# Kernel tuning notes

Measured on AMD Instinct MI355X. Metric: run time of the kernel, lower is better.

## Reference

```python
import jax, jax.numpy as jnp
import numpy as np

BEAM_WIDTH = 16   # beam_width init kwarg
TOP_PATHS = 1     # top_paths init kwarg
NEG = -1.0e30     # log-domain 'zero' (avoid -inf for stable grads)


def _beam_search_single(log_probs):
    """CTC prefix beam search for one example.

    log_probs: (T, V) log-softmax scores; blank is class V-1 (TF convention).
    Returns (decoded, scores): decoded (TOP_PATHS, T) int32 padded with -1,
    scores (TOP_PATHS,) final log-probabilities of the top prefixes.
    Prefix merging is done for the blank/repeat (stay) transitions of each
    beam (the dominant merge in CTC); cross-beam duplicate-prefix merging is
    approximated by pruning, as in common production beam-search kernels.
    """
    T, V = log_probs.shape
    C = V - 1                      # number of non-blank characters
    W = BEAM_WIDTH

    prefixes = jnp.full((W, T), -1, dtype=jnp.int32)
    lengths = jnp.zeros((W,), dtype=jnp.int32)
    p_b = jnp.full((W,), NEG, dtype=log_probs.dtype).at[0].set(0.0)   # log P(prefix, ends in blank)
    p_nb = jnp.full((W,), NEG, dtype=log_probs.dtype)                 # log P(prefix, ends in non-blank)

    def step(state, lp):
        prefixes, lengths, p_b, p_nb = state
        lp_blank = lp[C]
        lp_c = lp[:C]                                   # (C,)
        p_tot = jnp.logaddexp(p_b, p_nb)                # (W,)

        # last character of each beam (-1 if empty prefix)
        last = jnp.take_along_axis(prefixes, jnp.maximum(lengths - 1, 0)[:, None], axis=1)[:, 0]
        last = jnp.where(lengths > 0, last, -1)

        # --- stay candidates: same prefix, via blank or repeated last char ---
        new_p_b = p_tot + lp_blank                      # (W,)
        lp_last = jnp.take(lp_c, jnp.maximum(last, 0))
        new_p_nb_stay = jnp.where(last >= 0, p_nb + lp_last, NEG)
        stay_score = jnp.logaddexp(new_p_b, new_p_nb_stay)

        # --- extend candidates: prefix + c, for every non-blank c ---
        same = jnp.arange(C)[None, :] == last[:, None]  # (W, C)
        base = jnp.where(same, p_b[:, None], p_tot[:, None])
        ext_score = base + lp_c[None, :]                # (W, C) -> new p_nb

        all_scores = jnp.concatenate([stay_score, ext_score.reshape(-1)])  # (W + W*C,)
        top_scores, top_idx = jax.lax.top_k(all_scores, W)

        is_stay = top_idx < W
        beam = jnp.where(is_stay, top_idx, (top_idx - W) // C)
        char = jnp.where(is_stay, 0, (top_idx - W) % C).astype(jnp.int32)

        par_pref = prefixes[beam]                       # (W, T)
        par_len = lengths[beam]                         # (W,)
        pos = jnp.arange(T)[None, :]
        ext_pref = jnp.where(pos == par_len[:, None], char[:, None], par_pref)

        new_prefixes = jnp.where(is_stay[:, None], par_pref, ext_pref)
        new_lengths = jnp.where(is_stay, par_len, par_len + 1)
        new_pb = jnp.where(is_stay, new_p_b[beam], NEG)
        new_pnb = jnp.where(is_stay, new_p_nb_stay[beam], top_scores)
        return (new_prefixes, new_lengths, new_pb, new_pnb), None

    (prefixes, lengths, p_b, p_nb), _ = jax.lax.scan(step, (prefixes, lengths, p_b, p_nb), log_probs)

    final_scores = jnp.logaddexp(p_b, p_nb)             # (W,)
    best_scores, best_idx = jax.lax.top_k(final_scores, TOP_PATHS)
    return prefixes[best_idx], best_scores


def setup_inputs() -> dict:
    key = jax.random.key(0)
    # (batch, time, num_classes) logits, blank = last class (TF convention)
    inputs = jax.random.normal(key, (512, 512, 96), dtype=jnp.float32)
    return {"inputs": inputs}


def reference(inputs):
    # tf.nn.ctc_beam_search_decoder normalizes logits internally
    log_probs = jax.nn.log_softmax(inputs, axis=-1)        # (B, T, V)
    decoded, scores = jax.vmap(_beam_search_single)(log_probs)
    # decoded: (B, TOP_PATHS, T) token ids padded with -1 (stands in for the
    # string-table detokenize); probability = exp(log_probability) as in call()
    probability = jnp.exp(scores)                          # (B, TOP_PATHS)
    return decoded, probability
```

## Files before the change

### kernel.cpp

```cpp
#include <hip/hip_runtime.h>
#include <math.h>

#define NBATCH 512
#define TSTEPS 512
#define VCLS   96
#define CCLS   95
#define BWID   16
#define VPAD   104
#define NEGF   (-1e30f)

typedef unsigned long long u64;
typedef unsigned int u32;

__device__ __forceinline__ float exp_xla(float x){
    x = fminf(x, 88.3762626647950f);
    x = fmaxf(x, -88.3762626647949f);
    float t = __fadd_rn(__fmul_rn(x, 1.44269504088896341f), 0.5f);
    float m = floorf(t);
    float r = __fadd_rn(__fmul_rn(m, -0.693359375f), x);
    r = __fadd_rn(__fmul_rn(m, 2.12194440e-4f), r);
    float y = 1.9875691500E-4f;
    y = __fadd_rn(__fmul_rn(y, r), 1.3981999507E-3f);
    y = __fadd_rn(__fmul_rn(y, r), 8.3334519073E-3f);
    y = __fadd_rn(__fmul_rn(y, r), 4.1665795894E-2f);
    y = __fadd_rn(__fmul_rn(y, r), 1.6666665459E-1f);
    y = __fadd_rn(__fmul_rn(y, r), 5.0000001201E-1f);
    float r2 = __fmul_rn(r, r);
    y = __fadd_rn(__fmul_rn(y, r2), r);
    y = __fadd_rn(y, 1.0f);
    int n = (int)m;
    unsigned sb = (unsigned)(n + 127);
    float s = __uint_as_float(sb << 23);
    return __fmul_rn(y, s);
}

__device__ __forceinline__ float log_xla(float x){
    unsigned bits = __float_as_uint(x);
    int e = (int)(bits >> 23) - 126;
    float m = __uint_as_float((bits & 0x007FFFFFu) | 0x3F000000u);
    if (m < 0.707106781186547524f){
        e -= 1;
        m = __fsub_rn(__fadd_rn(m, m), 1.0f);
    } else {
        m = __fsub_rn(m, 1.0f);
    }
    float z = __fmul_rn(m, m);
    float p = 7.0376836292E-2f;
    p = __fadd_rn(__fmul_rn(p, m), -1.1514610310E-1f);
    p = __fadd_rn(__fmul_rn(p, m),  1.1676998740E-1f);
    p = __fadd_rn(__fmul_rn(p, m), -1.2420140846E-1f);
    p = __fadd_rn(__fmul_rn(p, m),  1.4249322787E-1f);
    p = __fadd_rn(__fmul_rn(p, m), -1.6668057665E-1f);
    p = __fadd_rn(__fmul_rn(p, m),  2.0000714765E-1f);
    p = __fadd_rn(__fmul_rn(p, m), -2.4999993993E-1f);
    p = __fadd_rn(__fmul_rn(p, m),  3.3333331174E-1f);
    float y = __fmul_rn(m, __fmul_rn(z, p));
    float fe = (float)e;
    y = __fadd_rn(y, __fmul_rn(-2.12194440e-4f, fe));
    y = __fadd_rn(y, __fmul_rn(-0.5f, z));
    float rr = __fadd_rn(m, y);
    rr = __fadd_rn(rr, __fmul_rn(0.693359375f, fe));
    return rr;
}

__device__ __forceinline__ float log1p_xla(float x){
    float u = __fadd_rn(x, 1.0f);
    if (u == 1.0f) return x;
    float lu = log_xla(u);
    float um1 = __fsub_rn(u, 1.0f);
    return __fmul_rn(lu, __fdiv_rn(x, um1));
}

__device__ __forceinline__ float logaddexp_x(float x, float y){
    float amax = fmaxf(x, y);
    float d = __fsub_rn(x, y);
    float e = exp_xla(-fabsf(d));
    float l1p = log1p_xla(e);
    return __fadd_rn(amax, l1p);
}

__device__ __forceinline__ unsigned ford(float f){
    unsigned u = __float_as_uint(f);
    return (u & 0x80000000u) ? ~u : (u | 0x80000000u);
}
__device__ __forceinline__ float unford(u32 u){
    return __uint_as_float((u & 0x80000000u) ? (u ^ 0x80000000u) : ~u);
}

__device__ __forceinline__ double packkey(float sc, int k){
    u64 kb = ((u64)ford(sc) << 31) | ((u64)((~(u32)k) & 0x7FFu) << 20);
    return __longlong_as_double((long long)kb);
}
__device__ __forceinline__ int decodekey(double wk){
    u32 idxinv = (u32)((u64)__double_as_longlong(wk) >> 20) & 0x7FFu;
    return (int)((~idxinv) & 0x7FFu);
}
__device__ __forceinline__ double packlp(float v, int c){
    u64 kb = ((u64)ford(v) << 31) | ((u64)((~(u32)c) & 0x7Fu) << 24);
    return __longlong_as_double((long long)kb);
}

__device__ __forceinline__ void wave_fence(){
    asm volatile("s_waitcnt lgkmcnt(0)" ::: "memory");
    __builtin_amdgcn_sched_barrier(0);
}

template<int CTRL>
__device__ __forceinline__ double dmaxd(double v){
    long long x = __double_as_longlong(v);
    int lo = __builtin_amdgcn_update_dpp((int)(u32)x, (int)(u32)x, CTRL, 0xF, 0xF, false);
    int hi = __builtin_amdgcn_update_dpp((int)(u32)(x >> 32), (int)(u32)(x >> 32), CTRL, 0xF, 0xF, false);
    double o = __longlong_as_double((long long)(((u64)(u32)hi << 32) | (u32)lo));
    return fmax(v, o);
}
template<int CTRL>
__device__ __forceinline__ float dmaxf(float v){
    int o = __builtin_amdgcn_update_dpp(__float_as_int(v), __float_as_int(v), CTRL, 0xF, 0xF, false);
    return fmaxf(v, __int_as_float(o));
}
__device__ __forceinline__ double rowmax_d(double v){
    v = dmaxd<0xB1>(v);
    v = dmaxd<0x4E>(v);
    v = dmaxd<0x141>(v);
    v = dmaxd<0x140>(v);
    return v;
}
__device__ __forceinline__ float rowmax_f(float v){
    v = dmaxf<0xB1>(v);
    v = dmaxf<0x4E>(v);
    v = dmaxf<0x141>(v);
    v = dmaxf<0x140>(v);
    return v;
}

__global__ __launch_bounds__(128)
void ctc_beam(const float* __restrict__ in, float* __restrict__ out)
{
    __shared__ __align__(16) float ring[8][2][VPAD];
    __shared__ __align__(8)  float2 srtS[8][2][17];
    __shared__ __align__(16) float evS[4][VPAD];
    __shared__ float lsS[4];
    __shared__ float2 stateF2[2][BWID];
    __shared__ int2   lastlenS[2][BWID];
    __shared__ unsigned short bp[2][TSTEPS][BWID];
    __shared__ float finalsS[2][BWID];

    const int tid  = threadIdx.x;
    const int wid  = tid >> 6;
    const int lane = tid & 63;
    const int rl   = lane & 15;
    const int eh   = (lane >> 4) & 1;
    const int bm   = rl;
    const int unit = lane >> 4;
    const int pex  = unit & 1;
    const int pdt  = unit >> 1;
    const int bex  = blockIdx.x * 2 + eh;
    const int pbex = blockIdx.x * 2 + pex;
    const float* __restrict__ prow = in + (size_t)pbex * TSTEPS * VCLS;

    float pb_r = NEGF, pnb_r = NEGF;
    int last_r = -1, len_r = 0;

    float xv[6], xw[6];

    auto LOADROW = [&](int r, float* dst){
        const float* p = prow + (size_t)r * VCLS + rl;
        #pragma unroll
        for (int j = 0; j < 6; ++j) dst[j] = p[j * 16];
    };
    auto PRODUCE = [&](int buf, const float* x){
        float lm = fmaxf(fmaxf(fmaxf(x[0], x[1]), fmaxf(x[2], x[3])), fmaxf(x[4], x[5]));
        float m = rowmax_f(lm);
        float sh[6];
        #pragma unroll
        for (int j = 0; j < 6; ++j){
            sh[j] = __fsub_rn(x[j], m);
            evS[unit][j * 16 + rl] = exp_xla(sh[j]);
        }
        wave_fence();
        if (rl == 0){
            float s = 0.0f;
            const float4* e4 = (const float4*)evS[unit];
            #pragma unroll
            for (int g = 0; g < 24; ++g){
                float4 w = e4[g];
                s = __fadd_rn(s, w.x); s = __fadd_rn(s, w.y);
                s = __fadd_rn(s, w.z); s = __fadd_rn(s, w.w);
            }
            lsS[unit] = log_xla(s);
        }
        wave_fence();
        float ls = lsS[unit];
        double kk[6];
        #pragma unroll
        for (int j = 0; j < 6; ++j){
            float lp = __fsub_rn(sh[j], ls);
            ring[buf][pex][j * 16 + rl] = lp;
            int c = j * 16 + rl;
            kk[j] = (c == CCLS) ? 0.0 : packlp(lp, c);
        }
        double t0 = fmax(kk[0], kk[1]), t1 = fmax(kk[2], kk[3]), t2 = fmax(kk[4], kk[5]);
        double pl = fmax(fmax(t0, t1), t2);
        #pragma unroll 1
        for (int i = 0; i < 17; ++i){
            double wk = rowmax_d(pl);
            if (rl == 0){
                u64 bits = (u64)__double_as_longlong(wk);
                int c = (int)((~(u32)(bits >> 24)) & 0x7Fu);
                srtS[buf][pex][i] = make_float2(unford((u32)(bits >> 31)), __int_as_float(c));
            }
            long long wkb = __double_as_longlong(wk);
            #pragma unroll
            for (int j = 0; j < 6; ++j)
                kk[j] = (__double_as_longlong(kk[j]) == wkb) ? 0.0 : kk[j];
            double u0 = fmax(kk[0], kk[1]), u1 = fmax(kk[2], kk[3]), u2 = fmax(kk[4], kk[5]);
            pl = fmax(fmax(u0, u1), u2);
        }
    };

    if (wid == 1){
        LOADROW(pdt, xv);
        PRODUCE(pdt, xv);
        LOADROW(2 + pdt, xv);
        PRODUCE(2 + pdt, xv);
        LOADROW(4 + pdt, xv);
        LOADROW(6 + pdt, xw);
    } else {
        pb_r = (bm == 0) ? 0.0f : NEGF;
        pnb_r = NEGF; last_r = -1; len_r = 0;
        if (lane < 32){
            lastlenS[eh][bm] = make_int2(-1, 0);
        }
    }
    __syncthreads();

    auto STEP = [&](int t){
        const float*  __restrict__ lpc = ring[t & 7][eh];
        const float2* __restrict__ srt = srtS[t & 7][eh];

        float lpb = lpc[CCLS];
        float lpl = lpc[(last_r >= 0) ? last_r : 0];
        float pt  = logaddexp_x(pb_r, pnb_r);
        float npb = pt + lpb;
        float stnb = (last_r >= 0) ? (pnb_r + lpl) : NEGF;
        float stay = logaddexp_x(npb, stnb);
        if (lane < 32){
            stateF2[eh][bm] = make_float2(npb, stnb);
        }

        const int idx0 = BWID + bm * CCLS;
        double ins = (last_r >= 0) ? packkey(__fadd_rn(pb_r, lpl), idx0 + last_r) : 0.0;
        double st[16];
        {
            float2 e0 = srt[0];
            int c0 = __float_as_int(e0.y);
            double raw_c = packkey(__fadd_rn(pt, e0.x), idx0 + c0);
            bool seen = (c0 == last_r);
            bool gtprev = true;
            double flt_prev = 0.0;
            #pragma unroll
            for (int j = 0; j < 16; ++j){
                float2 en = srt[j + 1];
                int cn = __float_as_int(en.y);
                double raw_n = packkey(__fadd_rn(pt, en.x), idx0 + cn);
                double flt_j = seen ? raw_n : raw_c;
                bool gt = (flt_j > ins);
                st[j] = gt ? flt_j : (gtprev ? ins : flt_prev);
                gtprev = gt; flt_prev = flt_j;
                raw_c = raw_n;
                seen = seen | (cn == last_r);
            }
        }

        #pragma unroll
        for (int p = 0; p < 2; ++p){
            #pragma unroll
            for (int j = 0; j < 15; ++j){
                double a = st[j], bk = st[j + 1];
                bool sw = a < bk;
                st[j]     = sw ? bk : a;
                st[j + 1] = sw ? a : bk;
            }
        }

        double stay_k = packkey(stay, bm);
        int mysel = 0;
        float myscore = 0.0f;
        #pragma unroll
        for (int r = 0; r < BWID; ++r){
            double loc = fmax(stay_k, st[0]);
            double wk = rowmax_d(loc);
            if (bm == r){
                mysel = decodekey(wk);
                myscore = unford((u32)((u64)__double_as_longlong(wk) >> 31));
            }
            if (r < BWID - 1){
                long long wkb = __double_as_longlong(wk);
                bool winstay = (__double_as_longlong(stay_k) == wkb);
                bool winst   = (__double_as_longlong(st[0]) == wkb);
                stay_k = winstay ? 0.0 : stay_k;
                #pragma unroll
                for (int j = 0; j < BWID - 1 - r; ++j) st[j] = winst ? st[j + 1] : st[j];
            }
        }

        wave_fence();
        int nlast, nlen, parent, code;
        float npbV, npnbV;
        {
            int s = mysel;
            if (s < BWID){
                parent = s; code = 0;
                float2 f2 = stateF2[eh][s];
                int2 i2 = lastlenS[eh][s];
                nlast = i2.x; nlen = i2.y;
                npbV = f2.x; npnbV = f2.y;
            } else {
                u32 e = (u32)(s - BWID);
                parent = (int)((e * 44151u) >> 22);
                int c = (int)(e - (u32)parent * 95u);
                code = c + 1;
                nlast = c;
                int2 i2 = lastlenS[eh][parent];
                nlen = i2.y + 1;
                npbV = NEGF;
                npnbV = myscore;
            }
        }
        __builtin_amdgcn_sched_barrier(0);
        pb_r = npbV; pnb_r = npnbV; last_r = nlast; len_r = nlen;
        if (lane < 32){
            lastlenS[eh][bm] = make_int2(nlast, nlen);
            bp[eh][t][bm] = (unsigned short)((parent << 8) | code);
        }
    };

    for (int k = 0; k < TSTEPS / 4; ++k){
        if (wid == 1){
            if (k + 1 < TSTEPS / 4){
                float cx[6], cy[6];
                #pragma unroll
                for (int j = 0; j < 6; ++j){ cx[j] = xv[j]; cy[j] = xw[j]; }
                if (k + 2 < TSTEPS / 4){
                    LOADROW(4 * k + 8 + pdt, xv);
                    LOADROW(4 * k + 10 + pdt, xw);
                }
                #pragma unroll 1
                for (int s = 0; s < 2; ++s){
                    float cc[6];
                    #pragma unroll
                    for (int j = 0; j < 6; ++j) cc[j] = s ? cy[j] : cx[j];
                    PRODUCE((4 * k + 4 + 2 * s + pdt) & 7, cc);
                }
            }
        } else {
            #pragma unroll 1
            for (int s = 0; s < 4; ++s) STEP(4 * k + s);
        }
        __syncthreads();
    }

    if (wid == 0){
        if (lane < 32) finalsS[eh][bm] = logaddexp_x(pb_r, pnb_r);
        wave_fence();
        int bi_loc = 0;
        if (rl == 0 && lane < 32){
            float bv = finalsS[eh][0];
            for (int i = 1; i < BWID; ++i){
                if (finalsS[eh][i] > bv){ bv = finalsS[eh][i]; bi_loc = i; }
            }
            out[(size_t)NBATCH * TSTEPS + bex] = exp_xla(bv);
        }
        int biA = __builtin_amdgcn_readlane(bi_loc, 0);
        int biB = __builtin_amdgcn_readlane(bi_loc, 16);
        int bi = eh ? biB : biA;
        int L  = lastlenS[eh][bi].y;
        if (lane < 32){
            for (int j = L + rl; j < TSTEPS; j += 16) out[(size_t)bex * TSTEPS + j] = -1.0f;
        }
        if (rl == 0 && lane < 32){
            int beam = bi, pos = L;
            for (int t = TSTEPS - 1; t >= 0; --t){
                unsigned short e = bp[eh][t][beam];
                int code = e & 0xFF;
                if (code){ out[(size_t)bex * TSTEPS + (pos - 1)] = (float)(code - 1); pos--; }
                beam = e >> 8;
            }
        }
    }
}

extern "C" void kernel_launch(void* const* d_in, const int* in_sizes, int n_in,
                              void* d_out, int out_size, void* d_ws, size_t ws_size,
                              hipStream_t stream)
{
    const float* in = (const float*)d_in[0];
    float* out = (float*)d_out;
    hipLaunchKernelGGL(ctc_beam, dim3(NBATCH / 2), dim3(128), 0, stream, in, out);
}
```

Before: 1.654 ms.

## Extract top-two per round in beam top-k merge, halving DPP reduction rounds

Result: slower. 1.702 ms (+2.9%).

```diff
diff --git a/kernel.cpp b/kernel.cpp
--- a/kernel.cpp
+++ b/kernel.cpp
@@ -106,11 +106,15 @@
 }
 
 template<int CTRL>
-__device__ __forceinline__ double dmaxd(double v){
+__device__ __forceinline__ double dpp_d(double v){
     long long x = __double_as_longlong(v);
     int lo = __builtin_amdgcn_update_dpp((int)(u32)x, (int)(u32)x, CTRL, 0xF, 0xF, false);
     int hi = __builtin_amdgcn_update_dpp((int)(u32)(x >> 32), (int)(u32)(x >> 32), CTRL, 0xF, 0xF, false);
-    double o = __longlong_as_double((long long)(((u64)(u32)hi << 32) | (u32)lo));
+    return __longlong_as_double((long long)(((u64)(u32)hi << 32) | (u32)lo));
+}
+template<int CTRL>
+__device__ __forceinline__ double dmaxd(double v){
+    double o = dpp_d<CTRL>(v);
     return fmax(v, o);
 }
 template<int CTRL>
@@ -119,18 +123,20 @@
     return fmaxf(v, __int_as_float(o));
 }
 __device__ __forceinline__ double rowmax_d(double v){
-    v = dmaxd<0xB1>(v);
-    v = dmaxd<0x4E>(v);
-    v = dmaxd<0x141>(v);
-    v = dmaxd<0x140>(v);
+    v = dmaxd<0xB1>(v); v = dmaxd<0x4E>(v); v = dmaxd<0x141>(v); v = dmaxd<0x140>(v);
     return v;
 }
 __device__ __forceinline__ float rowmax_f(float v){
-    v = dmaxf<0xB1>(v);
-    v = dmaxf<0x4E>(v);
-    v = dmaxf<0x141>(v);
-    v = dmaxf<0x140>(v);
+    v = dmaxf<0xB1>(v); v = dmaxf<0x4E>(v); v = dmaxf<0x141>(v); v = dmaxf<0x140>(v);
     return v;
+}
+template<int CTRL>
+__device__ __forceinline__ void dmax2(double& a1, double& a2){
+    double p1 = dpp_d<CTRL>(a1);
+    double p2 = dpp_d<CTRL>(a2);
+    double n1 = fmax(a1, p1);
+    double n2 = fmax(fmin(a1, p1), fmax(a2, p2));
+    a1 = n1; a2 = n2;
 }
 
 __global__ __launch_bounds__(128)
@@ -238,8 +244,15 @@
         const float*  __restrict__ lpc = ring[t & 7][eh];
         const float2* __restrict__ srt = srtS[t & 7][eh];
 
+        float sv[17]; int scv[17];
+        #pragma unroll
+        for (int j = 0; j < 17; ++j){
+            float2 e = srt[j];
+            sv[j] = e.x; scv[j] = __float_as_int(e.y);
+        }
         float lpb = lpc[CCLS];
         float lpl = lpc[(last_r >= 0) ? last_r : 0];
+
         float pt  = logaddexp_x(pb_r, pnb_r);
         float npb = pt + lpb;
         float stnb = (last_r >= 0) ? (pnb_r + lpl) : NEGF;
@@ -250,32 +263,35 @@
 
         const int idx0 = BWID + bm * CCLS;
         double ins = (last_r >= 0) ? packkey(__fadd_rn(pb_r, lpl), idx0 + last_r) : 0.0;
-        double st[16];
+        double raw[17];
+        #pragma unroll
+        for (int j = 0; j < 17; ++j)
+            raw[j] = packkey(__fadd_rn(pt, sv[j]), idx0 + scv[j]);
+        u32 mq = 0;
+        #pragma unroll
+        for (int j = 0; j < 17; ++j) mq |= (scv[j] == last_r) ? (1u << j) : 0u;
+        int tpos = mq ? __builtin_ctz(mq) : 99;
+        double st[18];
         {
-            float2 e0 = srt[0];
-            int c0 = __float_as_int(e0.y);
-            double raw_c = packkey(__fadd_rn(pt, e0.x), idx0 + c0);
-            bool seen = (c0 == last_r);
-            bool gtprev = true;
-            double flt_prev = 0.0;
+            double f0 = (0 < tpos) ? raw[0] : raw[1];
+            bool g0 = f0 > ins;
+            st[0] = g0 ? f0 : ins;
+            bool gprev = g0;
+            double fprev = f0;
             #pragma unroll
-            for (int j = 0; j < 16; ++j){
-                float2 en = srt[j + 1];
-                int cn = __float_as_int(en.y);
-                double raw_n = packkey(__fadd_rn(pt, en.x), idx0 + cn);
-                double flt_j = seen ? raw_n : raw_c;
-                bool gt = (flt_j > ins);
-                st[j] = gt ? flt_j : (gtprev ? ins : flt_prev);
-                gtprev = gt; flt_prev = flt_j;
-                raw_c = raw_n;
-                seen = seen | (cn == last_r);
-            }
-        }
-
-        #pragma unroll
-        for (int p = 0; p < 2; ++p){
+            for (int j = 1; j < 16; ++j){
+                double fj = (j < tpos) ? raw[j] : raw[j + 1];
+                bool g = fj > ins;
+                st[j] = g ? fj : (gprev ? ins : fprev);
+                gprev = g; fprev = fj;
+            }
+        }
+        st[16] = 0.0; st[17] = 0.0;
+
+        #pragma unroll
+        for (int ph = 0; ph < 4; ++ph){
             #pragma unroll
-            for (int j = 0; j < 15; ++j){
+            for (int j = (ph & 1); j < 15; j += 2){
                 double a = st[j], bk = st[j + 1];
                 bool sw = a < bk;
                 st[j]     = sw ? bk : a;
@@ -284,23 +300,38 @@
         }
 
         double stay_k = packkey(stay, bm);
+        double l1 = fmax(stay_k, st[0]);
+        double l2 = fmax(fmin(stay_k, st[0]), st[1]);
         int mysel = 0;
         float myscore = 0.0f;
         #pragma unroll
-        for (int r = 0; r < BWID; ++r){
-            double loc = fmax(stay_k, st[0]);
-            double wk = rowmax_d(loc);
-            if (bm == r){
-                mysel = decodekey(wk);
-                myscore = unford((u32)((u64)__double_as_longlong(wk) >> 31));
-            }
-            if (r < BWID - 1){
-                long long wkb = __double_as_longlong(wk);
-                bool winstay = (__double_as_longlong(stay_k) == wkb);
-                bool winst   = (__double_as_longlong(st[0]) == wkb);
-                stay_k = winstay ? 0.0 : stay_k;
+        for (int r = 0; r < 8; ++r){
+            double a1 = l1, a2 = l2;
+            dmax2<0xB1>(a1, a2);
+            dmax2<0x4E>(a1, a2);
+            dmax2<0x141>(a1, a2);
+            dmax2<0x140>(a1, a2);
+            if (bm == 2 * r){
+                mysel = decodekey(a1);
+                myscore = unford((u32)((u64)__double_as_longlong(a1) >> 31));
+            }
+            if (bm == 2 * r + 1){
+                mysel = decodekey(a2);
+                myscore = unford((u32)((u64)__double_as_longlong(a2) >> 31));
+            }
+            if (r < 7){
+                long long w1 = __double_as_longlong(a1);
+                long long w2 = __double_as_longlong(a2);
+                bool m0 = (__double_as_longlong(st[0]) == w1) | (__double_as_longlong(st[0]) == w2);
+                bool m1 = (__double_as_longlong(st[1]) == w1) | (__double_as_longlong(st[1]) == w2);
+                int cnt = (int)m0 + (int)m1;
                 #pragma unroll
-                for (int j = 0; j < BWID - 1 - r; ++j) st[j] = winst ? st[j + 1] : st[j];
+                for (int j = 0; j < 16; ++j)
+                    st[j] = (cnt == 0) ? st[j] : ((cnt == 1) ? st[j + 1] : st[j + 2]);
+                bool sm = (__double_as_longlong(stay_k) == w1) | (__double_as_longlong(stay_k) == w2);
+                stay_k = sm ? 0.0 : stay_k;
+                l1 = fmax(stay_k, st[0]);
+                l2 = fmax(fmin(stay_k, st[0]), st[1]);
             }
         }
 
```
